# Optimization experiments

Hardware: AMD Instinct MI355X
Metric: run time of the kernel (lower is better)

Reference implementation:

```python
import jax, jax.numpy as jnp
import numpy as np

N = 50000
E = 1000000


def _edge_sage(x, edge_attr, src, dst, Wn, bn, Ws, bs):
    # message: lin_neigh(concat(x_j, edge_attr)); x_j = x[src] (PyG source_to_target)
    msg = jnp.concatenate([x[src], edge_attr], axis=-1) @ Wn + bn  # [E+N, out]
    agg = jax.ops.segment_sum(msg, dst, num_segments=x.shape[0])
    cnt = jax.ops.segment_sum(jnp.ones((dst.shape[0],), msg.dtype), dst,
                              num_segments=x.shape[0])
    mean = agg / cnt[:, None]  # self-loops guarantee cnt >= 1
    return jax.nn.relu(x @ Ws + bs + mean)


def setup_inputs() -> dict:
    key = jax.random.key(0)
    ks = jax.random.split(key, 12)
    din, dedge, dh, dout = 64, 16, 64, 64
    s = lambda f: 1.0 / np.sqrt(f)
    return {
        "x": jax.random.normal(ks[0], (N, din), jnp.float32),
        "edge_index": jax.random.randint(ks[1], (2, E), 0, N, jnp.int32),
        "edge_attr": jax.random.normal(ks[2], (E, dedge), jnp.float32),
        "W1n": jax.random.uniform(ks[3], (din + dedge, dh), jnp.float32, -s(din + dedge), s(din + dedge)),
        "b1n": jax.random.uniform(ks[4], (dh,), jnp.float32, -s(din + dedge), s(din + dedge)),
        "W1s": jax.random.uniform(ks[5], (din, dh), jnp.float32, -s(din), s(din)),
        "b1s": jax.random.uniform(ks[6], (dh,), jnp.float32, -s(din), s(din)),
        "W2n": jax.random.uniform(ks[7], (dh + dedge, dout), jnp.float32, -s(dh + dedge), s(dh + dedge)),
        "b2n": jax.random.uniform(ks[8], (dout,), jnp.float32, -s(dh + dedge), s(dh + dedge)),
        "W2s": jax.random.uniform(ks[9], (dh, dout), jnp.float32, -s(dh), s(dh)),
        "b2s": jax.random.uniform(ks[10], (dout,), jnp.float32, -s(dh), s(dh)),
    }


def reference(x, edge_index, edge_attr, W1n, b1n, W1s, b1s, W2n, b2n, W2s, b2s):
    n = x.shape[0]
    loops = jnp.arange(n, dtype=edge_index.dtype)
    src = jnp.concatenate([edge_index[0], loops])
    dst = jnp.concatenate([edge_index[1], loops])
    ea = jnp.concatenate(
        [edge_attr, jnp.zeros((n, edge_attr.shape[1]), edge_attr.dtype)], axis=0)
    h = _edge_sage(x, ea, src, dst, W1n, b1n, W1s, b1s)
    return _edge_sage(h, ea, src, dst, W2n, b2n, W2s, b2s)
```

## Files before the change

kernel.cpp:

```cpp
#include <hip/hip_runtime.h>

#define N_NODES 50000
#define NE 1000000
#define NBUK 196
#define CHUNK 4096
#define MAXBE 6144

typedef float vfloat4 __attribute__((ext_vector_type(4)));
typedef unsigned short ushort4v __attribute__((ext_vector_type(4)));
typedef unsigned short ushort8v __attribute__((ext_vector_type(8)));

__device__ __forceinline__ unsigned short f2b(float f) {
  unsigned u = __float_as_uint(f);
  u += 0x7FFF + ((u >> 16) & 1);
  return (unsigned short)(u >> 16);
}
__device__ __forceinline__ float b2f(unsigned short h) {
  return __uint_as_float(((unsigned)h) << 16);
}



__global__ __launch_bounds__(256) void bucket_count(
    const int* __restrict__ ei, int* __restrict__ BCNT) {
  __shared__ int c[256];
  int t = threadIdx.x;
  c[t] = 0;
  __syncthreads();
  int i0 = blockIdx.x * CHUNK;
  int n = min(CHUNK, NE - i0);
  for (int i = t; i < n; i += 256)
    atomicAdd(&c[ei[NE + i0 + i] >> 8], 1);
  __syncthreads();
  if (t < NBUK && c[t] > 0) atomicAdd(&BCNT[t], c[t]);
}

__global__ __launch_bounds__(256) void scan_buckets(
    const int* __restrict__ BCNT, int* __restrict__ BOFF,
    int* __restrict__ BCUR, int* __restrict__ OFF) {
  __shared__ int s[256];
  int t = threadIdx.x;
  int v = (t < NBUK) ? BCNT[t] : 0;
  s[t] = v;
  __syncthreads();
  #pragma unroll
  for (int off = 1; off < 256; off <<= 1) {
    int u = (t >= off) ? s[t - off] : 0;
    __syncthreads();
    s[t] += u;
    __syncthreads();
  }
  int ex = s[t] - v;
  if (t < NBUK) { BOFF[t] = ex; BCUR[t] = ex; }
  if (t == NBUK - 1) BOFF[NBUK] = s[t];
  if (t == 0) OFF[N_NODES] = NE;
}

__global__ __launch_bounds__(256) void bucket_scatter(
    const int* __restrict__ ei, int* __restrict__ BCUR,
    long long* __restrict__ BKT) {
  __shared__ int cnt[256], sscan[256], base[256], cur[256], gb[256];
  __shared__ long long binned[CHUNK];
  __shared__ unsigned short dstl[CHUNK];
  int t = threadIdx.x;
  int c0 = blockIdx.x * CHUNK;
  int n = min(CHUNK, NE - c0);
  cnt[t] = 0;
  __syncthreads();
  for (int i = t; i < n; i += 256) {
    int dst = ei[NE + c0 + i];
    atomicAdd(&cnt[dst >> 8], 1);
  }
  __syncthreads();
  int myc = cnt[t];
  sscan[t] = myc;
  __syncthreads();
  #pragma unroll
  for (int off = 1; off < 256; off <<= 1) {
    int u = (t >= off) ? sscan[t - off] : 0;
    __syncthreads();
    sscan[t] += u;
    __syncthreads();
  }
  base[t] = sscan[t] - myc;
  cur[t] = sscan[t] - myc;
  if (myc > 0) gb[t] = atomicAdd(&BCUR[t], myc);
  __syncthreads();
  for (int i = t; i < n; i += 256) {
    int src = ei[c0 + i];
    int dst = ei[NE + c0 + i];
    int b = dst >> 8;
    int lp = atomicAdd(&cur[b], 1);
    binned[lp] = ((long long)(c0 + i) << 25) | ((long long)src << 8)
               | (long long)(dst & 255);
    dstl[lp] = (unsigned short)dst;
  }
  __syncthreads();
  for (int i = t; i < n; i += 256) {
    int b = ((int)dstl[i]) >> 8;
    __builtin_nontemporal_store(binned[i], &BKT[gb[b] + (i - base[b])]);
  }
}

__global__ __launch_bounds__(1024) void bucket_sort(
    const long long* __restrict__ BKT, const int* __restrict__ BOFF,
    int* __restrict__ OFF, long long* __restrict__ SRT) {
  __shared__ int cnt[256], ss[256], loff[256], cur[256];
  __shared__ long long buf[MAXBE];
  int t = threadIdx.x;
  if (t < 256) { cnt[t] = 0; cur[t] = 0; }
  __syncthreads();
  int b = blockIdx.x;
  int s0 = BOFF[b], s1 = BOFF[b + 1];
  int n = s1 - s0;
  for (int i = t; i < n; i += 1024) {
    long long pl = __builtin_nontemporal_load(&BKT[s0 + i]);
    if (i < MAXBE) buf[i] = pl;
    atomicAdd(&cnt[(int)(pl & 255)], 1);
  }
  __syncthreads();
  if (t < 256) ss[t] = cnt[t];
  __syncthreads();
  #pragma unroll
  for (int off = 1; off < 256; off <<= 1) {
    int u = 0;
    if (t < 256 && t >= off) u = ss[t - off];
    __syncthreads();
    if (t < 256) ss[t] += u;
    __syncthreads();
  }
  if (t < 256) loff[t] = ss[t] - cnt[t];
  __syncthreads();
  int nb0 = b << 8;
  if (t < 256 && nb0 + t < N_NODES) OFF[nb0 + t] = s0 + loff[t];
  for (int i = t; i < n; i += 1024) {
    long long pl = (i < MAXBE) ? buf[i] : __builtin_nontemporal_load(&BKT[s0 + i]);
    int dl = (int)(pl & 255);
    int p = atomicAdd(&cur[dl], 1);
    SRT[s0 + loff[dl] + p] = pl;
  }
}

__global__ __launch_bounds__(256) void conv_bf16(
    const float* __restrict__ in, unsigned short* __restrict__ out) {
  int i = blockIdx.x * 256 + threadIdx.x;
  if (i >= (N_NODES * 64) / 4) return;
  vfloat4 v = ((const vfloat4*)in)[i];
  ushort4v o = { f2b(v[0]), f2b(v[1]), f2b(v[2]), f2b(v[3]) };
  ((ushort4v*)out)[i] = o;
}

template <bool HAS_EA>
__global__ __launch_bounds__(256) void gather_agg(
    const unsigned short* __restrict__ XB,
    const float* __restrict__ ea,
    const long long* __restrict__ SRT, const int* __restrict__ OFF,
    float* __restrict__ AGG,
    float* __restrict__ AEout)
{
  int w = (blockIdx.x * 256 + threadIdx.x) >> 6;
  int lane = threadIdx.x & 63;
  if (w >= N_NODES) return;
  int s0 = OFF[w], s1 = OFF[w + 1];
  int slot = lane >> 3;
  int j = lane & 7;
  float ax[8] = {0.f,0.f,0.f,0.f,0.f,0.f,0.f,0.f};
  float ae0=0.f, ae1=0.f, ae2=0.f, ae3=0.f;
  for (int p = s0 + slot; p < s1; p += 8) {
    long long pl = __builtin_nontemporal_load(&SRT[p]);
    int src = (int)((pl >> 8) & 0x1FFFF);
    ushort8v v = ((const ushort8v*)XB)[src * 8 + j];
    #pragma unroll
    for (int k = 0; k < 8; ++k) ax[k] += b2f(v[k]);
    if (HAS_EA) {
      int eid = (int)(pl >> 25);
      if (j < 4) {
        vfloat4 ev = __builtin_nontemporal_load((const vfloat4*)(ea + eid * 16 + j * 4));
        ae0 += ev[0]; ae1 += ev[1]; ae2 += ev[2]; ae3 += ev[3];
      }
    }
  }
  #pragma unroll
  for (int m = 8; m <= 32; m <<= 1) {
    #pragma unroll
    for (int k = 0; k < 8; ++k) ax[k] += __shfl_xor(ax[k], m, 64);
    if (HAS_EA) {
      ae0 += __shfl_xor(ae0, m, 64);
      ae1 += __shfl_xor(ae1, m, 64);
      ae2 += __shfl_xor(ae2, m, 64);
      ae3 += __shfl_xor(ae3, m, 64);
    }
  }
  if (lane < 8) {
    vfloat4 o0 = {ax[0], ax[1], ax[2], ax[3]};
    vfloat4 o1 = {ax[4], ax[5], ax[6], ax[7]};
    __builtin_nontemporal_store(o0, (vfloat4*)(AGG + w * 64 + lane * 8));
    __builtin_nontemporal_store(o1, (vfloat4*)(AGG + w * 64 + lane * 8 + 4));
  }
  if (HAS_EA && lane < 4) {
    vfloat4 oe = {ae0, ae1, ae2, ae3};
    __builtin_nontemporal_store(oe, (vfloat4*)(AEout + w * 16 + lane * 4));
  }
}

template <bool XBF, bool OBF>
__global__ __launch_bounds__(256) void layer_kernel(
    const void* __restrict__ xin_, const float* __restrict__ AGG,
    const float* __restrict__ AE, const int* __restrict__ OFF,
    const float* __restrict__ Ws, const float* __restrict__ bs,
    const float* __restrict__ Wn, const float* __restrict__ bn,
    void* __restrict__ out_)
{
  __shared__ float Ml[144][68];
  __shared__ float Wl[72][64];
  __shared__ float biasl[64];
  __shared__ float invl[64];

  const float* xf = (const float*)xin_;
  const unsigned short* xb = (const unsigned short*)xin_;

  int t = threadIdx.x;
  int base = blockIdx.x * 64;

  if (t < 64) {
    int i = base + t;
    float deg = (i < N_NODES) ? (float)(OFF[i + 1] - OFF[i]) : 0.0f;
    invl[t] = 1.0f / (deg + 1.0f);
    biasl[t] = bs[t] + bn[t];
  }
  __syncthreads();

  for (int idx = t; idx < 4096; idx += 256) {
    int r = idx >> 6, k = idx & 63;
    int i = base + r;
    float xv = 0.f, av = 0.f;
    if (i < N_NODES) {
      xv = XBF ? b2f(xb[i * 64 + k]) : xf[i * 64 + k];
      av = AGG[i * 64 + k];
    }
    Ml[k][r] = xv;
    Ml[64 + k][r] = (av + xv) * invl[r];
  }
  for (int idx = t; idx < 1024; idx += 256) {
    int r = idx >> 4, k = idx & 15;
    int i = base + r;
    Ml[128 + k][r] = (i < N_NODES) ? AE[i * 16 + k] * invl[r] : 0.0f;
  }

  int tx = t & 15;
  int ty = t >> 4;
  float acc[4][4] = {{0.f}};

  for (int kc = 0; kc < 2; ++kc) {
    for (int idx = t; idx < 72 * 64; idx += 256) {
      int lr = idx >> 6, c = idx & 63;
      int k = kc * 72 + lr;
      Wl[lr][c] = (k < 64) ? Ws[k * 64 + c] : Wn[(k - 64) * 64 + c];
    }
    __syncthreads();
    #pragma unroll 8
    for (int k = 0; k < 72; ++k) {
      float4 a = *(const float4*)&Ml[kc * 72 + k][ty * 4];
      float4 b = *(const float4*)&Wl[k][tx * 4];
      float av[4] = {a.x, a.y, a.z, a.w};
      float bv[4] = {b.x, b.y, b.z, b.w};
      #pragma unroll
      for (int ri = 0; ri < 4; ++ri)
        #pragma unroll
        for (int ci = 0; ci < 4; ++ci)
          acc[ri][ci] = fmaf(av[ri], bv[ci], acc[ri][ci]);
    }
    __syncthreads();
  }

  #pragma unroll
  for (int ri = 0; ri < 4; ++ri) {
    int i = base + ty * 4 + ri;
    if (i < N_NODES) {
      float o0 = fmaxf(acc[ri][0] + biasl[tx * 4 + 0], 0.0f);
      float o1 = fmaxf(acc[ri][1] + biasl[tx * 4 + 1], 0.0f);
      float o2 = fmaxf(acc[ri][2] + biasl[tx * 4 + 2], 0.0f);
      float o3 = fmaxf(acc[ri][3] + biasl[tx * 4 + 3], 0.0f);
      if (OBF) {
        ushort4v ob = { f2b(o0), f2b(o1), f2b(o2), f2b(o3) };
        ((ushort4v*)out_)[i * 16 + tx] = ob;
      } else {
        float4 of = {o0, o1, o2, o3};
        ((float4*)out_)[i * 16 + tx] = of;
      }
    }
  }
}

extern "C" void kernel_launch(void* const* d_in, const int* in_sizes, int n_in,
                              void* d_out, int out_size, void* d_ws, size_t ws_size,
                              hipStream_t stream) {
  const float* x   = (const float*)d_in[0];
  const int*   ei  = (const int*)d_in[1];
  const float* ea  = (const float*)d_in[2];
  const float* W1n = (const float*)d_in[3];
  const float* b1n = (const float*)d_in[4];
  const float* W1s = (const float*)d_in[5];
  const float* b1s = (const float*)d_in[6];
  const float* W2n = (const float*)d_in[7];
  const float* b2n = (const float*)d_in[8];
  const float* W2s = (const float*)d_in[9];
  const float* b2s = (const float*)d_in[10];

  int* wsi = (int*)d_ws;
  float* wsf = (float*)d_ws;
  int*  OFF  = wsi;
  long long* SRT = (long long*)(wsi + 50004);
  unsigned short* XB = (unsigned short*)(wsi + 2050004);
  float* AE  = wsf + 3650004;
  int*  BCNT = wsi + 4450004;
  int*  BOFF = wsi + 4450260;
  int*  BCUR = wsi + 4450516;
  long long* BKT = (long long*)(wsi + 4450772);
  float* AGG = (float*)d_out;
  float* out = (float*)d_out;

  hipMemsetAsync(BCNT, 0, 256 * 4, stream);

  int cb = (NE + CHUNK - 1) / CHUNK;
  bucket_count<<<cb, 256, 0, stream>>>(ei, BCNT);
  scan_buckets<<<1, 256, 0, stream>>>(BCNT, BOFF, BCUR, OFF);
  bucket_scatter<<<cb, 256, 0, stream>>>(ei, BCUR, BKT);
  bucket_sort<<<NBUK, 1024, 0, stream>>>(BKT, BOFF, OFF, SRT);
  conv_bf16<<<(N_NODES * 64 / 4 + 255) / 256, 256, 0, stream>>>(x, XB);

  gather_agg<true><<<12500, 256, 0, stream>>>(XB, ea, SRT, OFF, AGG, AE);
  layer_kernel<false, true><<<782, 256, 0, stream>>>(
      x, AGG, AE, OFF, W1s, b1s, W1n, b1n, XB);
  gather_agg<false><<<12500, 256, 0, stream>>>(XB, nullptr, SRT, OFF, AGG, nullptr);
  layer_kernel<true, false><<<782, 256, 0, stream>>>(
      XB, AGG, AE, OFF, W2s, b2s, W2n, b2n, out);
}
```

Measured before the change: 217.0 us.

## Split edge gather into two source-half passes for L2 locality

The bucket sort now partitions each node's incoming edges by whether the source index falls in the lower or upper half of the node range, and records a mid offset per node. Each gather is then run as two launches, each touching only half of the bf16 feature table, so the random source reads fit better in cache. The second pass reads back and accumulates the partial sums, which costs extra launches, extra AGG/AE traffic and a second read of edge metadata and offsets.

```diff
diff --git a/kernel.cpp b/kernel.cpp
--- a/kernel.cpp
+++ b/kernel.cpp
@@ -18,7 +18,6 @@
 __device__ __forceinline__ float b2f(unsigned short h) {
   return __uint_as_float(((unsigned)h) << 16);
 }
-
 
 
 __global__ __launch_bounds__(256) void bucket_count(
@@ -104,11 +103,11 @@
 
 __global__ __launch_bounds__(1024) void bucket_sort(
     const long long* __restrict__ BKT, const int* __restrict__ BOFF,
-    int* __restrict__ OFF, long long* __restrict__ SRT) {
-  __shared__ int cnt[256], ss[256], loff[256], cur[256];
+    int* __restrict__ OFF, int* __restrict__ OFFH, long long* __restrict__ SRT) {
+  __shared__ int cnt0[256], cnt1[256], ss[256], loff[256], cur0[256], cur1[256];
   __shared__ long long buf[MAXBE];
   int t = threadIdx.x;
-  if (t < 256) { cnt[t] = 0; cur[t] = 0; }
+  if (t < 256) { cnt0[t] = 0; cnt1[t] = 0; cur0[t] = 0; cur1[t] = 0; }
   __syncthreads();
   int b = blockIdx.x;
   int s0 = BOFF[b], s1 = BOFF[b + 1];
@@ -116,10 +115,13 @@
   for (int i = t; i < n; i += 1024) {
     long long pl = __builtin_nontemporal_load(&BKT[s0 + i]);
     if (i < MAXBE) buf[i] = pl;
-    atomicAdd(&cnt[(int)(pl & 255)], 1);
-  }
-  __syncthreads();
-  if (t < 256) ss[t] = cnt[t];
+    int dl = (int)(pl & 255);
+    int src = (int)((pl >> 8) & 0x1FFFF);
+    if (src < N_NODES / 2) atomicAdd(&cnt0[dl], 1);
+    else                   atomicAdd(&cnt1[dl], 1);
+  }
+  __syncthreads();
+  if (t < 256) ss[t] = cnt0[t] + cnt1[t];
   __syncthreads();
   #pragma unroll
   for (int off = 1; off < 256; off <<= 1) {
@@ -129,15 +131,21 @@
     if (t < 256) ss[t] += u;
     __syncthreads();
   }
-  if (t < 256) loff[t] = ss[t] - cnt[t];
+  if (t < 256) loff[t] = ss[t] - (cnt0[t] + cnt1[t]);
   __syncthreads();
   int nb0 = b << 8;
-  if (t < 256 && nb0 + t < N_NODES) OFF[nb0 + t] = s0 + loff[t];
+  if (t < 256 && nb0 + t < N_NODES) {
+    OFF[nb0 + t] = s0 + loff[t];
+    OFFH[nb0 + t] = s0 + loff[t] + cnt0[t];
+  }
   for (int i = t; i < n; i += 1024) {
     long long pl = (i < MAXBE) ? buf[i] : __builtin_nontemporal_load(&BKT[s0 + i]);
     int dl = (int)(pl & 255);
-    int p = atomicAdd(&cur[dl], 1);
-    SRT[s0 + loff[dl] + p] = pl;
+    int src = (int)((pl >> 8) & 0x1FFFF);
+    int pos;
+    if (src < N_NODES / 2) pos = s0 + loff[dl] + atomicAdd(&cur0[dl], 1);
+    else                   pos = s0 + loff[dl] + cnt0[dl] + atomicAdd(&cur1[dl], 1);
+    SRT[pos] = pl;
   }
 }
 
@@ -150,18 +158,20 @@
   ((ushort4v*)out)[i] = o;
 }
 
-template <bool HAS_EA>
+template <bool HAS_EA, int HALF>
 __global__ __launch_bounds__(256) void gather_agg(
     const unsigned short* __restrict__ XB,
     const float* __restrict__ ea,
     const long long* __restrict__ SRT, const int* __restrict__ OFF,
+    const int* __restrict__ OFFH,
     float* __restrict__ AGG,
     float* __restrict__ AEout)
 {
   int w = (blockIdx.x * 256 + threadIdx.x) >> 6;
   int lane = threadIdx.x & 63;
   if (w >= N_NODES) return;
-  int s0 = OFF[w], s1 = OFF[w + 1];
+  int s0 = HALF ? OFFH[w] : OFF[w];
+  int s1 = HALF ? OFF[w + 1] : OFFH[w];
   int slot = lane >> 3;
   int j = lane & 7;
   float ax[8] = {0.f,0.f,0.f,0.f,0.f,0.f,0.f,0.f};
@@ -194,11 +204,20 @@
   if (lane < 8) {
     vfloat4 o0 = {ax[0], ax[1], ax[2], ax[3]};
     vfloat4 o1 = {ax[4], ax[5], ax[6], ax[7]};
+    if (HALF) {
+      vfloat4 p0 = *(const vfloat4*)(AGG + w * 64 + lane * 8);
+      vfloat4 p1 = *(const vfloat4*)(AGG + w * 64 + lane * 8 + 4);
+      o0 += p0; o1 += p1;
+    }
     __builtin_nontemporal_store(o0, (vfloat4*)(AGG + w * 64 + lane * 8));
     __builtin_nontemporal_store(o1, (vfloat4*)(AGG + w * 64 + lane * 8 + 4));
   }
   if (HAS_EA && lane < 4) {
     vfloat4 oe = {ae0, ae1, ae2, ae3};
+    if (HALF) {
+      vfloat4 pe = *(const vfloat4*)(AEout + w * 16 + lane * 4);
+      oe += pe;
+    }
     __builtin_nontemporal_store(oe, (vfloat4*)(AEout + w * 16 + lane * 4));
   }
 }
@@ -310,13 +329,14 @@
   int* wsi = (int*)d_ws;
   float* wsf = (float*)d_ws;
   int*  OFF  = wsi;
-  long long* SRT = (long long*)(wsi + 50004);
-  unsigned short* XB = (unsigned short*)(wsi + 2050004);
-  float* AE  = wsf + 3650004;
-  int*  BCNT = wsi + 4450004;
-  int*  BOFF = wsi + 4450260;
-  int*  BCUR = wsi + 4450516;
-  long long* BKT = (long long*)(wsi + 4450772);
+  int*  OFFH = wsi + 50004;
+  long long* SRT = (long long*)(wsi + 100004);
+  unsigned short* XB = (unsigned short*)(wsi + 2100004);
+  float* AE  = wsf + 3700004;
+  int*  BCNT = wsi + 4500004;
+  int*  BOFF = wsi + 4500260;
+  int*  BCUR = wsi + 4500516;
+  long long* BKT = (long long*)(wsi + 4500772);
   float* AGG = (float*)d_out;
   float* out = (float*)d_out;
 
@@ -326,13 +346,15 @@
   bucket_count<<<cb, 256, 0, stream>>>(ei, BCNT);
   scan_buckets<<<1, 256, 0, stream>>>(BCNT, BOFF, BCUR, OFF);
   bucket_scatter<<<cb, 256, 0, stream>>>(ei, BCUR, BKT);
-  bucket_sort<<<NBUK, 1024, 0, stream>>>(BKT, BOFF, OFF, SRT);
+  bucket_sort<<<NBUK, 1024, 0, stream>>>(BKT, BOFF, OFF, OFFH, SRT);
   conv_bf16<<<(N_NODES * 64 / 4 + 255) / 256, 256, 0, stream>>>(x, XB);
 
-  gather_agg<true><<<12500, 256, 0, stream>>>(XB, ea, SRT, OFF, AGG, AE);
+  gather_agg<true, 0><<<12500, 256, 0, stream>>>(XB, ea, SRT, OFF, OFFH, AGG, AE);
+  gather_agg<true, 1><<<12500, 256, 0, stream>>>(XB, ea, SRT, OFF, OFFH, AGG, AE);
   layer_kernel<false, true><<<782, 256, 0, stream>>>(
       x, AGG, AE, OFF, W1s, b1s, W1n, b1n, XB);
-  gather_agg<false><<<12500, 256, 0, stream>>>(XB, nullptr, SRT, OFF, AGG, nullptr);
+  gather_agg<false, 0><<<12500, 256, 0, stream>>>(XB, nullptr, SRT, OFF, OFFH, AGG, nullptr);
+  gather_agg<false, 1><<<12500, 256, 0, stream>>>(XB, nullptr, SRT, OFF, OFFH, AGG, nullptr);
   layer_kernel<true, false><<<782, 256, 0, stream>>>(
       XB, AGG, AE, OFF, W2s, b2s, W2n, b2n, out);
 }
```

New measurement: 246.8 us. 1.14x slower.
